# Performance work log

Measured on AMD Instinct MI355X. Metric: run time of the kernel, lower is better.

## Reference

```python
import jax, jax.numpy as jnp
from jax import lax
import numpy as np

LATENT = 256
FLAT = 128 * 28 * 28  # 100352


def _conv(x, w, b, stride):
    # PyTorch Conv2d(k=3, stride, padding=1) in NCHW/OIHW
    y = lax.conv_general_dilated(x, w, (stride, stride), ((1, 1), (1, 1)),
                                 dimension_numbers=('NCHW', 'OIHW', 'NCHW'))
    return y + b[None, :, None, None]


def _deconv(x, w, b):
    # PyTorch ConvTranspose2d(k=3, stride=2, padding=1, output_padding=1).
    # w has PyTorch layout [in, out, kh, kw]; flip spatially + swap io -> OIHW.
    wt = jnp.flip(w, (2, 3)).transpose(1, 0, 2, 3)
    y = lax.conv_general_dilated(x, wt, (1, 1), ((1, 2), (1, 2)),
                                 lhs_dilation=(2, 2),
                                 dimension_numbers=('NCHW', 'OIHW', 'NCHW'))
    return y + b[None, :, None, None]


def _self_attn(x, wq, bq, wk, bk, wv, bv, gamma):
    # Full spatial self-attention over N = H*W tokens (the headroom hotspot).
    B, C, H, W = x.shape
    N = H * W
    xf = x.reshape(B, C, N)
    q = jnp.einsum('oc,bcn->bno', wq, xf) + bq            # [B, N, C//8]
    k = jnp.einsum('oc,bcn->bon', wk, xf) + bk[None, :, None]  # [B, C//8, N]
    attn = jax.nn.softmax(jnp.einsum('bno,bom->bnm', q, k), axis=-1)  # [B,N,N]
    v = jnp.einsum('oc,bcn->bon', wv, xf) + bv[None, :, None]  # [B, C, N]
    out = jnp.einsum('bcn,bmn->bcm', v, attn).reshape(B, C, H, W)
    return gamma * out + x


def setup_inputs() -> dict:
    key = jax.random.key(0)
    ks = iter(jax.random.split(key, 40))
    n = lambda shape, s=0.05: jax.random.normal(next(ks), shape, dtype=jnp.float32) * s
    inp = {
        'x': jax.random.normal(next(ks), (1, 3, 224, 224), dtype=jnp.float32),
        'eps': jax.random.normal(next(ks), (1, LATENT), dtype=jnp.float32),
        'conv1_w': n((32, 3, 3, 3)), 'conv1_b': n((32,)),
        'q1_w': n((4, 32)), 'q1_b': n((4,)),
        'k1_w': n((4, 32)), 'k1_b': n((4,)),
        'v1_w': n((32, 32)), 'v1_b': n((32,)),
        'gamma1': jnp.full((1,), 0.1, dtype=jnp.float32),
        'conv2_w': n((64, 32, 3, 3)), 'conv2_b': n((64,)),
        'q2_w': n((8, 64)), 'q2_b': n((8,)),
        'k2_w': n((8, 64)), 'k2_b': n((8,)),
        'v2_w': n((64, 64)), 'v2_b': n((64,)),
        'gamma2': jnp.full((1,), 0.1, dtype=jnp.float32),
        'conv3_w': n((128, 64, 3, 3)), 'conv3_b': n((128,)),
        'fc_mu_w': n((FLAT, LATENT), 0.01), 'fc_mu_b': n((LATENT,)),
        'fc_lv_w': n((FLAT, LATENT), 0.01), 'fc_lv_b': n((LATENT,)),
        'fc_dec_w': n((LATENT, FLAT), 0.01), 'fc_dec_b': n((FLAT,)),
        'dc1_w': n((128, 64, 3, 3)), 'dc1_b': n((64,)),
        'dc2_w': n((64, 32, 3, 3)), 'dc2_b': n((32,)),
        'dc3_w': n((32, 3, 3, 3)), 'dc3_b': n((3,)),
    }
    return inp


def reference(x, eps, conv1_w, conv1_b, q1_w, q1_b, k1_w, k1_b, v1_w, v1_b, gamma1,
              conv2_w, conv2_b, q2_w, q2_b, k2_w, k2_b, v2_w, v2_b, gamma2,
              conv3_w, conv3_b, fc_mu_w, fc_mu_b, fc_lv_w, fc_lv_b,
              fc_dec_w, fc_dec_b, dc1_w, dc1_b, dc2_w, dc2_b, dc3_w, dc3_b):
    B = x.shape[0]
    h = jax.nn.relu(_conv(x, conv1_w, conv1_b, 2))          # [B,32,112,112]
    h = _self_attn(h, q1_w, q1_b, k1_w, k1_b, v1_w, v1_b, gamma1)
    h = jax.nn.relu(_conv(h, conv2_w, conv2_b, 2))          # [B,64,56,56]
    h = _self_attn(h, q2_w, q2_b, k2_w, k2_b, v2_w, v2_b, gamma2)
    h = jax.nn.relu(_conv(h, conv3_w, conv3_b, 2))          # [B,128,28,28]
    hf = h.reshape(B, FLAT)
    mu = hf @ fc_mu_w + fc_mu_b
    logvar = hf @ fc_lv_w + fc_lv_b
    z = mu + eps * jnp.exp(0.5 * logvar)                    # reparametrize
    d = jax.nn.relu(z @ fc_dec_w + fc_dec_b).reshape(B, 128, 28, 28)
    d = jax.nn.relu(_deconv(d, dc1_w, dc1_b))               # [B,64,56,56]
    d = jax.nn.relu(_deconv(d, dc2_w, dc2_b))               # [B,32,112,112]
    recon = jax.nn.sigmoid(_deconv(d, dc3_w, dc3_b))        # [B,3,224,224]
    return recon, mu, logvar
```

## Files before the change

kernel.cpp:

```cpp
#include <hip/hip_runtime.h>
#include <hip/hip_bf16.h>

typedef __hip_bfloat16 bf16;
typedef __attribute__((ext_vector_type(8))) short short8v;
typedef __attribute__((ext_vector_type(4))) float f32x4;

__device__ __forceinline__ unsigned int cvtpk(float lo, float hi){
  unsigned int r;
  asm volatile("v_cvt_pk_bf16_f32 %0, %1, %2" : "=v"(r) : "v"(lo), "v"(hi));
  return r;
}
__device__ __forceinline__ float exp2a(float x){
  float r;
  asm volatile("v_exp_f32 %0, %1" : "=v"(r) : "v"(x));
  return r;
}

template<int CIN>
__global__ __launch_bounds__(256) void k_conv_s2t(const float* __restrict__ in, const float* __restrict__ w,
    const float* __restrict__ bias, float* __restrict__ out, int Hin, int Win){
  const int Hout = Hin>>1, Wout = Win>>1, HW = Hout*Wout;
  __shared__ float wl[CIN*9];
  const int oc = blockIdx.y, tid = threadIdx.x;
  for(int i=tid;i<CIN*9;i+=256) wl[i] = w[oc*CIN*9 + i];
  __syncthreads();
  const int idx = blockIdx.x*256 + tid;
  if(idx >= HW) return;
  const int oy = idx/Wout, ox = idx - oy*Wout;
  const int iy0 = 2*oy-1, ix0 = 2*ox-1;
  const float mt = iy0>=0 ? 1.f:0.f, ml = ix0>=0 ? 1.f:0.f;
  const int iyc = iy0<0?0:iy0, ixc = ix0<0?0:ix0;
  const int x1 = ix0+1, x2 = ix0+2;
  float acc = bias[oc];
  #pragma unroll 4
  for(int ic=0; ic<CIN; ++ic){
    const float* b0 = in + (ic*Hin + iyc )*Win;
    const float* b1 = in + (ic*Hin + iy0+1)*Win;
    const float* b2 = in + (ic*Hin + iy0+2)*Win;
    const float* wp = wl + ic*9;
    float t00 = b0[ixc]*(mt*ml), t01 = b0[x1]*mt, t02 = b0[x2]*mt;
    float t10 = b1[ixc]*ml,      t11 = b1[x1],    t12 = b1[x2];
    float t20 = b2[ixc]*ml,      t21 = b2[x1],    t22 = b2[x2];
    acc += t00*wp[0]+t01*wp[1]+t02*wp[2]
         + t10*wp[3]+t11*wp[4]+t12*wp[5]
         + t20*wp[6]+t21*wp[7]+t22*wp[8];
  }
  out[oc*HW + idx] = fmaxf(acc, 0.f);
}

template<int C, int O, int TPN>
__global__ __launch_bounds__(256) void k_qkv(const float* __restrict__ x,
    const float* __restrict__ wq, const float* __restrict__ bq,
    const float* __restrict__ wk, const float* __restrict__ bk,
    const float* __restrict__ wv, const float* __restrict__ bv,
    float* __restrict__ q, float* __restrict__ k, bf16* __restrict__ v, int N){
  constexpr int NPB = 256/TPN;
  constexpr int OP = O/TPN > 0 ? O/TPN : 1;
  constexpr int CP = C/TPN;
  const int n = blockIdx.x*NPB + threadIdx.x/TPN;
  const int p = threadIdx.x%TPN;
  float xc[C];
  #pragma unroll
  for(int c=0;c<C;++c) xc[c] = x[c*N+n];
  #pragma unroll
  for(int oo=0;oo<OP;++oo){
    int o = p*OP + oo;
    float aq = bq[o], ak = bk[o];
    #pragma unroll
    for(int c=0;c<C;++c){ aq += wq[o*C+c]*xc[c]; ak += wk[o*C+c]*xc[c]; }
    q[n*O+o] = aq;
    k[o*N+n] = ak;
  }
  #pragma unroll
  for(int cc=0;cc<CP;++cc){
    int o = p*CP + cc;
    float av = bv[o];
    #pragma unroll
    for(int c=0;c<C;++c) av += wv[o*C+c]*xc[c];
    v[o*N+n] = __float2bfloat16(av);
  }
}

template<int C, int O, int ST, int NSPLIT, int QG>
__global__ __launch_bounds__(256) void k_attn_mfma(
    const float* __restrict__ q, const float* __restrict__ kk, const bf16* __restrict__ vb,
    float* __restrict__ pacc, float* __restrict__ pden, int N){
  constexpr int NT = C/16;
  constexpr int OF4 = O/4;
  constexpr int VROW = ST*2 + 16;
  __shared__ __align__(16) char vsm[C*VROW];
  __shared__ float4 ksm4[(ST + ST/8)*OF4];
  const int tid = threadIdx.x;
  const int qblk = blockIdx.x / NSPLIT, split = blockIdx.x % NSPLIT;
  const int KEYS = N / NSPLIT;
  const int kbase = split * KEYS;
  const int wv = tid >> 6;
  const int l  = tid & 63;
  const int lg = l >> 4, lq = l & 15;
  const int qbase = qblk*(64*QG) + wv*(16*QG);
  float qv[QG][O];
  #pragma unroll
  for(int g=0; g<QG; ++g)
    #pragma unroll
    for(int o=0;o<O;++o) qv[g][o] = q[(qbase + g*16 + lq)*O + o] * 1.44269504f;
  f32x4 acc[QG][NT];
  #pragma unroll
  for(int g=0; g<QG; ++g)
    #pragma unroll
    for(int nt=0;nt<NT;++nt) acc[g][nt] = (f32x4){0.f,0.f,0.f,0.f};
  float den[QG];
  #pragma unroll
  for(int g=0; g<QG; ++g) den[g] = 0.f;

  for(int g0=0; g0<KEYS; g0+=ST){
    __syncthreads();
    for(int j=tid; j<ST; j+=256){
      int row = j + (j>>3);
      #pragma unroll
      for(int h=0;h<OF4;++h){
        float4 kv;
        ((float*)&kv)[0] = kk[(h*4+0)*N + kbase + g0 + j];
        ((float*)&kv)[1] = kk[(h*4+1)*N + kbase + g0 + j];
        ((float*)&kv)[2] = kk[(h*4+2)*N + kbase + g0 + j];
        ((float*)&kv)[3] = kk[(h*4+3)*N + kbase + g0 + j];
        ksm4[row*OF4 + h] = kv;
      }
    }
    for(int ch=tid; ch < C*(ST/8); ch += 256){
      int c = ch / (ST/8), j8 = ch % (ST/8);
      *(uint4*)(vsm + c*VROW + j8*16) =
          *(const uint4*)(vb + (size_t)c*N + kbase + g0 + j8*8);
    }
    __syncthreads();
    #pragma unroll
    for(int s=0; s<ST/32; ++s){
      float pr[QG][8];
      #pragma unroll
      for(int e=0; e<8; ++e){
        const int row = s*36 + lg*9 + e;
        #pragma unroll
        for(int g=0; g<QG; ++g){
          float sc = 0.f;
          #pragma unroll
          for(int h=0;h<OF4;++h){
            float4 k4 = ksm4[row*OF4 + h];
            sc += qv[g][h*4+0]*k4.x + qv[g][h*4+1]*k4.y + qv[g][h*4+2]*k4.z + qv[g][h*4+3]*k4.w;
          }
          pr[g][e] = exp2a(sc);
        }
      }
      union { unsigned int u[4]; short8v s8; } pa[QG];
      #pragma unroll
      for(int g=0; g<QG; ++g){
        #pragma unroll
        for(int u=0; u<4; ++u) pa[g].u[u] = cvtpk(pr[g][2*u], pr[g][2*u+1]);
        #pragma unroll
        for(int e=0; e<8; ++e) den[g] += pr[g][e];
      }
      #pragma unroll
      for(int nt=0; nt<NT; ++nt){
        short8v bf_ = *(const short8v*)(vsm + (lq + nt*16)*VROW + (s*32 + lg*8)*2);
        #pragma unroll
        for(int g=0; g<QG; ++g)
          acc[g][nt] = __builtin_amdgcn_mfma_f32_16x16x32_bf16(pa[g].s8, bf_, acc[g][nt], 0,0,0);
      }
    }
  }
  #pragma unroll
  for(int g=0; g<QG; ++g){
    den[g] += __shfl_xor(den[g], 16);
    den[g] += __shfl_xor(den[g], 32);
    if(lg == 0) pden[(size_t)split*N + qbase + g*16 + lq] = den[g];
  }
  #pragma unroll
  for(int g=0; g<QG; ++g)
    #pragma unroll
    for(int nt=0; nt<NT; ++nt)
      #pragma unroll
      for(int r=0;r<4;++r){
        int qg_ = qbase + g*16 + lg*4 + r;
        pacc[((size_t)split*N + qg_)*C + nt*16 + lq] = acc[g][nt][r];
      }
}

template<int C, int NSPLIT>
__global__ __launch_bounds__(256) void k_attn_comb(const float* __restrict__ pacc, const float* __restrict__ pden,
    const float* __restrict__ xin, const float* __restrict__ gamma, float* __restrict__ out, int N){
  int idx = blockIdx.x*256 + threadIdx.x;
  if(idx >= N*C) return;
  int c = idx / N, m = idx - c*N;
  float a = 0.f, d = 0.f;
  #pragma unroll
  for(int s=0;s<NSPLIT;++s){
    a += pacc[((size_t)s*N + m)*C + c];
    d += pden[(size_t)s*N + m];
  }
  out[idx] = gamma[0]*a/d + xin[idx];
}

__global__ __launch_bounds__(256) void k_fc2_part(const float* __restrict__ hf,
    const float* __restrict__ wmu, const float* __restrict__ wlv,
    float* __restrict__ pmu, float* __restrict__ plv){
  __shared__ float sh[64];
  __shared__ float4 red[4][64];
  const int t = threadIdx.x, blk = blockIdx.x, f0 = blk*64;
  const int w = t>>6, l = t&63;
  const float* wsel = blockIdx.y ? wlv : wmu;
  float*       dsel = blockIdx.y ? plv : pmu;
  if(t < 64) sh[t] = hf[f0+t];
  __syncthreads();
  const float4* wp = (const float4*)(wsel + (size_t)(f0 + w*16)*256) + l;
  f32x4 a = {0.f,0.f,0.f,0.f};
  #pragma unroll
  for(int r=0; r<16; ++r){
    float h = sh[w*16 + r];
    float4 u = wp[r*64];
    a[0] += h*u.x; a[1] += h*u.y; a[2] += h*u.z; a[3] += h*u.w;
  }
  red[w][l] = (float4){a[0],a[1],a[2],a[3]};
  __syncthreads();
  const float* rr = (const float*)red;
  dsel[(size_t)blk*256 + t] = rr[t] + rr[256+t] + rr[512+t] + rr[768+t];
}

__global__ __launch_bounds__(256) void k_reparam_p(const float* __restrict__ pmu, const float* __restrict__ plv,
    const float* __restrict__ bmu, const float* __restrict__ blv, const float* __restrict__ eps,
    float* __restrict__ z, float* __restrict__ omu, float* __restrict__ olv){
  const int o = blockIdx.x, t = threadIdx.x;
  __shared__ float rm[4], rl[4];
  float sm = 0.f, sl = 0.f;
  for(int j=t; j<1568; j+=256){ sm += pmu[(size_t)j*256+o]; sl += plv[(size_t)j*256+o]; }
  #pragma unroll
  for(int off=32; off>=1; off>>=1){ sm += __shfl_xor(sm, off); sl += __shfl_xor(sl, off); }
  if((t&63)==0){ rm[t>>6]=sm; rl[t>>6]=sl; }
  __syncthreads();
  if(t==0){
    float mu = bmu[o] + rm[0]+rm[1]+rm[2]+rm[3];
    float lv = blv[o] + rl[0]+rl[1]+rl[2]+rl[3];
    z[o] = mu + eps[o] * expf(0.5f*lv);
    omu[o] = mu;
    olv[o] = lv;
  }
}

template<int OSPL>
__global__ __launch_bounds__(256) void k_fc_dec_p(const float* __restrict__ z, const float* __restrict__ w,
    float* __restrict__ pfd){
  constexpr int OPC = 256/OSPL;
  __shared__ float sz[OPC];
  const int t = threadIdx.x, blk = blockIdx.x, os = blockIdx.y;
  if(t<OPC) sz[t] = z[os*OPC + t];
  __syncthreads();
  const size_t f4 = (size_t)blk*256 + t;
  const float4* wp = (const float4*)w + (size_t)os*OPC*25088 + f4;
  f32x4 a = {0.f,0.f,0.f,0.f};
  #pragma unroll 8
  for(int o=0;o<OPC;++o){
    float zz = sz[o];
    float4 u = wp[(size_t)o*25088];
    a[0] += zz*u.x; a[1] += zz*u.y; a[2] += zz*u.z; a[3] += zz*u.w;
  }
  ((float4*)pfd)[(size_t)os*25088 + f4] = (float4){a[0],a[1],a[2],a[3]};
}

template<int OSPL>
__global__ __launch_bounds__(256) void k_fc_dec_c(const float* __restrict__ pfd, const float* __restrict__ b,
    float* __restrict__ out){
  const int i = blockIdx.x*256 + threadIdx.x;
  const float4* p4 = (const float4*)pfd;
  float4 bb = ((const float4*)b)[i];
  f32x4 s = {bb.x, bb.y, bb.z, bb.w};
  #pragma unroll
  for(int k=0;k<OSPL;++k){
    float4 u = p4[(size_t)k*25088 + i];
    s[0] += u.x; s[1] += u.y; s[2] += u.z; s[3] += u.w;
  }
  ((float4*)out)[i] = (float4){fmaxf(s[0],0.f), fmaxf(s[1],0.f), fmaxf(s[2],0.f), fmaxf(s[3],0.f)};
}

template<int CIN, int COUT, int ACT>
__global__ __launch_bounds__(256) void k_deconv_p(const float* __restrict__ in, const float* __restrict__ w,
    const float* __restrict__ bias, float* __restrict__ out, int Hin, int Win){
  __shared__ float wl[CIN*9];
  const int oc = blockIdx.y;
  const int tid = threadIdx.x;
  for(int i=tid; i<CIN*9; i+=256) wl[i] = w[((i/9)*COUT + oc)*9 + (i%9)];
  __syncthreads();
  const int nq = Hin*Win;
  const int code = blockIdx.x*256 + tid;
  if(code >= 4*nq) return;
  const int q = code % nq;
  const int pcode = code / nq;
  const int px = pcode & 1, py = pcode >> 1;
  const int qy = q / Win, qx = q - qy*Win;
  const float m1x = (qx+1 < Win) ? 1.f : 0.f;
  const float m1y = (qy+1 < Hin) ? 1.f : 0.f;
  const int qxc = (qx+1 < Win) ? qx+1 : qx;
  const int qyc = (qy+1 < Hin) ? qy+1 : qy;
  const int o00 = qy*Win+qx, o01 = qy*Win+qxc, o10 = qyc*Win+qx, o11 = qyc*Win+qxc;
  const int HW = nq;
  float acc = bias[oc];
  if(pcode == 0){
    #pragma unroll 4
    for(int ic=0; ic<CIN; ++ic) acc += in[ic*HW + o00] * wl[ic*9+4];
  } else if(pcode == 1){
    #pragma unroll 4
    for(int ic=0; ic<CIN; ++ic){
      acc += in[ic*HW + o00] * wl[ic*9+5];
      acc += (in[ic*HW + o01]*m1x) * wl[ic*9+3];
    }
  } else if(pcode == 2){
    #pragma unroll 4
    for(int ic=0; ic<CIN; ++ic){
      acc += in[ic*HW + o00] * wl[ic*9+7];
      acc += (in[ic*HW + o10]*m1y) * wl[ic*9+1];
    }
  } else {
    #pragma unroll 4
    for(int ic=0; ic<CIN; ++ic){
      acc += in[ic*HW + o00] * wl[ic*9+8];
      acc += (in[ic*HW + o01]*m1x) * wl[ic*9+6];
      acc += (in[ic*HW + o10]*m1y) * wl[ic*9+2];
      acc += (in[ic*HW + o11]*(m1x*m1y)) * wl[ic*9+0];
    }
  }
  const int oy = 2*qy+py, ox = 2*qx+px;
  float r = (ACT==0) ? fmaxf(acc, 0.f) : 1.f/(1.f + __expf(-acc));
  out[(oc*2*Hin + oy)*2*Win + ox] = r;
}

extern "C" void kernel_launch(void* const* d_in, const int* in_sizes, int n_in,
                              void* d_out, int out_size, void* d_ws, size_t ws_size,
                              hipStream_t stream){
  const float* X    = (const float*)d_in[0];
  const float* EPS  = (const float*)d_in[1];
  const float* c1w  = (const float*)d_in[2];  const float* c1b = (const float*)d_in[3];
  const float* q1w  = (const float*)d_in[4];  const float* q1b = (const float*)d_in[5];
  const float* k1w  = (const float*)d_in[6];  const float* k1b = (const float*)d_in[7];
  const float* v1w  = (const float*)d_in[8];  const float* v1b = (const float*)d_in[9];
  const float* g1   = (const float*)d_in[10];
  const float* c2w  = (const float*)d_in[11]; const float* c2b = (const float*)d_in[12];
  const float* q2w  = (const float*)d_in[13]; const float* q2b = (const float*)d_in[14];
  const float* k2w  = (const float*)d_in[15]; const float* k2b = (const float*)d_in[16];
  const float* v2w  = (const float*)d_in[17]; const float* v2b = (const float*)d_in[18];
  const float* g2   = (const float*)d_in[19];
  const float* c3w  = (const float*)d_in[20]; const float* c3b = (const float*)d_in[21];
  const float* fmw  = (const float*)d_in[22]; const float* fmb = (const float*)d_in[23];
  const float* flw  = (const float*)d_in[24]; const float* flb = (const float*)d_in[25];
  const float* fdw  = (const float*)d_in[26]; const float* fdb = (const float*)d_in[27];
  const float* d1w  = (const float*)d_in[28]; const float* d1b = (const float*)d_in[29];
  const float* d2w  = (const float*)d_in[30]; const float* d2b = (const float*)d_in[31];
  const float* d3w  = (const float*)d_in[32]; const float* d3b = (const float*)d_in[33];

  float* ws  = (float*)d_ws;
  float* h1  = ws;
  float* h1a = h1  + 401408;
  float* q1  = h1a + 401408;
  float* k1  = q1  + 50176;
  float* v1f = k1  + 50176;
  float* h2  = v1f + 401408;
  float* h2a = h2  + 200704;
  float* q2  = h2a + 200704;
  float* k2  = q2  + 25088;
  float* v2f = k2  + 25088;
  float* h3  = v2f + 200704;
  float* z   = h3  + 100352 + 200704;
  float* part= h3  + 100352 + 200704 + 256;
  bf16* v1b_ = (bf16*)v1f;
  bf16* v2b_ = (bf16*)v2f;
  float* pmu = part;
  float* plv = part + 401408;
  float* pfd = part + 802816;
  float* dd0 = h1;
  float* dd1 = h1 + 100352;
  float* dd2 = h1a;

  const size_t base = 2258176;
  const bool big = ws_size >= (base + 2809856 + 87808) * 4;
  float* pdn = part + (big ? 2809856 : 802816);

  float* OUT = (float*)d_out;

  k_conv_s2t<3><<<dim3(49,32),dim3(256),0,stream>>>(X, c1w, c1b, h1, 224, 224);
  k_qkv<32,4,4><<<dim3(196),dim3(256),0,stream>>>(h1, q1w,q1b, k1w,k1b, v1w,v1b, q1,k1,v1b_, 12544);
  if(big){
    k_attn_mfma<32,4,128,7,2><<<dim3(686),dim3(256),0,stream>>>(q1,k1,v1b_, part, pdn, 12544);
    k_attn_comb<32,7><<<dim3(1568),dim3(256),0,stream>>>(part, pdn, h1, g1, h1a, 12544);
  } else {
    k_attn_mfma<32,4,128,2,2><<<dim3(196),dim3(256),0,stream>>>(q1,k1,v1b_, part, pdn, 12544);
    k_attn_comb<32,2><<<dim3(1568),dim3(256),0,stream>>>(part, pdn, h1, g1, h1a, 12544);
  }
  k_conv_s2t<32><<<dim3(13,64),dim3(256),0,stream>>>(h1a, c2w, c2b, h2, 112, 112);
  k_qkv<64,8,8><<<dim3(98),dim3(256),0,stream>>>(h2, q2w,q2b, k2w,k2b, v2w,v2b, q2,k2,v2b_, 3136);
  if(big){
    k_attn_mfma<64,8,64,7,1><<<dim3(343),dim3(256),0,stream>>>(q2,k2,v2b_, part, pdn, 3136);
    k_attn_comb<64,7><<<dim3(784),dim3(256),0,stream>>>(part, pdn, h2, g2, h2a, 3136);
  } else {
    k_attn_mfma<64,8,64,1,1><<<dim3(49),dim3(256),0,stream>>>(q2,k2,v2b_, part, pdn, 3136);
    k_attn_comb<64,1><<<dim3(784),dim3(256),0,stream>>>(part, pdn, h2, g2, h2a, 3136);
  }
  k_conv_s2t<64><<<dim3(4,128),dim3(256),0,stream>>>(h2a, c3w, c3b, h3, 56, 56);
  k_fc2_part<<<dim3(1568,2),dim3(256),0,stream>>>(h3, fmw, flw, pmu, plv);
  k_reparam_p<<<dim3(256),dim3(256),0,stream>>>(pmu, plv, fmb, flb, EPS, z, OUT+150528, OUT+150784);
  if(big){
    k_fc_dec_p<16><<<dim3(98,16),dim3(256),0,stream>>>(z, fdw, pfd);
    k_fc_dec_c<16><<<dim3(98),dim3(256),0,stream>>>(pfd, fdb, dd0);
  } else {
    k_fc_dec_p<4><<<dim3(98,4),dim3(256),0,stream>>>(z, fdw, pfd);
    k_fc_dec_c<4><<<dim3(98),dim3(256),0,stream>>>(pfd, fdb, dd0);
  }
  k_deconv_p<128,64,0><<<dim3(13,64),dim3(256),0,stream>>>(dd0, d1w, d1b, dd1, 28,28);
  k_deconv_p<64,32,0><<<dim3(49,32),dim3(256),0,stream>>>(dd1, d2w, d2b, dd2, 56,56);
  k_deconv_p<32,3,1><<<dim3(196,3),dim3(256),0,stream>>>(dd2, d3w, d3b, OUT, 112,112);
}
```

Before: 390.2 us.

## Double-buffer K/V tiles in attention and transpose combine through shared memory

The attention kernel now prefetches the next K/V tile into registers while the current tile is processed from a second shared-memory buffer, so each tile needs one barrier instead of two and global loads overlap with the MFMA/exp work. The combine kernel is rewritten to read partial accumulators contiguously, transpose them through an LDS tile, and write NCHW output coalesced, replacing the strided gathers. The inline asm also drops `volatile` so the compiler can schedule the exp and convert instructions. The costs are doubled LDS and extra registers held for the prefetch, which may lower occupancy.

```diff
diff --git a/kernel.cpp b/kernel.cpp
--- a/kernel.cpp
+++ b/kernel.cpp
@@ -7,12 +7,12 @@
 
 __device__ __forceinline__ unsigned int cvtpk(float lo, float hi){
   unsigned int r;
-  asm volatile("v_cvt_pk_bf16_f32 %0, %1, %2" : "=v"(r) : "v"(lo), "v"(hi));
+  asm("v_cvt_pk_bf16_f32 %0, %1, %2" : "=v"(r) : "v"(lo), "v"(hi));
   return r;
 }
 __device__ __forceinline__ float exp2a(float x){
   float r;
-  asm volatile("v_exp_f32 %0, %1" : "=v"(r) : "v"(x));
+  asm("v_exp_f32 %0, %1" : "=v"(r) : "v"(x));
   return r;
 }
 
@@ -88,8 +88,9 @@
   constexpr int NT = C/16;
   constexpr int OF4 = O/4;
   constexpr int VROW = ST*2 + 16;
-  __shared__ __align__(16) char vsm[C*VROW];
-  __shared__ float4 ksm4[(ST + ST/8)*OF4];
+  constexpr int VIT  = C*(ST/8)/256;
+  __shared__ __align__(16) char vsm[2][C*VROW];
+  __shared__ float4 ksm4[2][(ST + ST/8)*OF4];
   const int tid = threadIdx.x;
   const int qblk = blockIdx.x / NSPLIT, split = blockIdx.x % NSPLIT;
   const int KEYS = N / NSPLIT;
@@ -112,26 +113,48 @@
   #pragma unroll
   for(int g=0; g<QG; ++g) den[g] = 0.f;
 
-  for(int g0=0; g0<KEYS; g0+=ST){
-    __syncthreads();
-    for(int j=tid; j<ST; j+=256){
-      int row = j + (j>>3);
+  float4 kreg[OF4];
+  uint4  vreg[VIT];
+  const bool kact = tid < ST;
+
+  auto LOAD = [&](int g0){
+    if(kact){
       #pragma unroll
       for(int h=0;h<OF4;++h){
-        float4 kv;
-        ((float*)&kv)[0] = kk[(h*4+0)*N + kbase + g0 + j];
-        ((float*)&kv)[1] = kk[(h*4+1)*N + kbase + g0 + j];
-        ((float*)&kv)[2] = kk[(h*4+2)*N + kbase + g0 + j];
-        ((float*)&kv)[3] = kk[(h*4+3)*N + kbase + g0 + j];
-        ksm4[row*OF4 + h] = kv;
+        ((float*)&kreg[h])[0] = kk[(h*4+0)*N + kbase + g0 + tid];
+        ((float*)&kreg[h])[1] = kk[(h*4+1)*N + kbase + g0 + tid];
+        ((float*)&kreg[h])[2] = kk[(h*4+2)*N + kbase + g0 + tid];
+        ((float*)&kreg[h])[3] = kk[(h*4+3)*N + kbase + g0 + tid];
       }
     }
-    for(int ch=tid; ch < C*(ST/8); ch += 256){
-      int c = ch / (ST/8), j8 = ch % (ST/8);
-      *(uint4*)(vsm + c*VROW + j8*16) =
-          *(const uint4*)(vb + (size_t)c*N + kbase + g0 + j8*8);
-    }
-    __syncthreads();
+    #pragma unroll
+    for(int i=0;i<VIT;++i){
+      int ch = i*256 + tid;
+      int c = ch/(ST/8), j8 = ch%(ST/8);
+      vreg[i] = *(const uint4*)(vb + (size_t)c*N + kbase + g0 + j8*8);
+    }
+  };
+  auto STORE = [&](int b){
+    if(kact){
+      int row = tid + (tid>>3);
+      #pragma unroll
+      for(int h=0;h<OF4;++h) ksm4[b][row*OF4 + h] = kreg[h];
+    }
+    #pragma unroll
+    for(int i=0;i<VIT;++i){
+      int ch = i*256 + tid;
+      int c = ch/(ST/8), j8 = ch%(ST/8);
+      *(uint4*)(vsm[b] + c*VROW + j8*16) = vreg[i];
+    }
+  };
+
+  const int NTILE = KEYS/ST;
+  LOAD(0);
+  STORE(0);
+  __syncthreads();
+  int cur = 0;
+  for(int t=0; t<NTILE; ++t){
+    if(t+1 < NTILE) LOAD((t+1)*ST);
     #pragma unroll
     for(int s=0; s<ST/32; ++s){
       float pr[QG][8];
@@ -143,7 +166,7 @@
           float sc = 0.f;
           #pragma unroll
           for(int h=0;h<OF4;++h){
-            float4 k4 = ksm4[row*OF4 + h];
+            float4 k4 = ksm4[cur][row*OF4 + h];
             sc += qv[g][h*4+0]*k4.x + qv[g][h*4+1]*k4.y + qv[g][h*4+2]*k4.z + qv[g][h*4+3]*k4.w;
           }
           pr[g][e] = exp2a(sc);
@@ -159,12 +182,15 @@
       }
       #pragma unroll
       for(int nt=0; nt<NT; ++nt){
-        short8v bf_ = *(const short8v*)(vsm + (lq + nt*16)*VROW + (s*32 + lg*8)*2);
+        short8v bf_ = *(const short8v*)(vsm[cur] + (lq + nt*16)*VROW + (s*32 + lg*8)*2);
         #pragma unroll
         for(int g=0; g<QG; ++g)
           acc[g][nt] = __builtin_amdgcn_mfma_f32_16x16x32_bf16(pa[g].s8, bf_, acc[g][nt], 0,0,0);
       }
     }
+    if(t+1 < NTILE) STORE(cur^1);
+    __syncthreads();
+    cur ^= 1;
   }
   #pragma unroll
   for(int g=0; g<QG; ++g){
@@ -184,18 +210,38 @@
 }
 
 template<int C, int NSPLIT>
-__global__ __launch_bounds__(256) void k_attn_comb(const float* __restrict__ pacc, const float* __restrict__ pden,
-    const float* __restrict__ xin, const float* __restrict__ gamma, float* __restrict__ out, int N){
-  int idx = blockIdx.x*256 + threadIdx.x;
-  if(idx >= N*C) return;
-  int c = idx / N, m = idx - c*N;
-  float a = 0.f, d = 0.f;
-  #pragma unroll
-  for(int s=0;s<NSPLIT;++s){
-    a += pacc[((size_t)s*N + m)*C + c];
-    d += pden[(size_t)s*N + m];
-  }
-  out[idx] = gamma[0]*a/d + xin[idx];
+__global__ __launch_bounds__(256) void k_attn_combT(const float* __restrict__ pacc,
+    const float* __restrict__ pden, const float* __restrict__ xin,
+    const float* __restrict__ gamma, float* __restrict__ out, int N){
+  __shared__ float tl[C][65];
+  __shared__ float dl[64];
+  const int t = threadIdx.x;
+  const int m0 = blockIdx.x*64;
+  if(t < 64){
+    float d = 0.f;
+    #pragma unroll
+    for(int s=0;s<NSPLIT;++s) d += pden[(size_t)s*N + m0 + t];
+    dl[t] = d;
+  }
+  constexpr int E = 64*C/256;
+  #pragma unroll
+  for(int e=0;e<E;++e){
+    int f = e*256 + t;
+    int ml = f/C, c = f - ml*C;
+    float a = 0.f;
+    #pragma unroll
+    for(int s=0;s<NSPLIT;++s) a += pacc[(size_t)s*N*C + (size_t)m0*C + f];
+    tl[c][ml] = a;
+  }
+  __syncthreads();
+  const float gm = gamma[0];
+  #pragma unroll
+  for(int e=0;e<E;++e){
+    int f = e*256 + t;
+    int c = f>>6, ml = f & 63;
+    size_t gi = (size_t)c*N + m0 + ml;
+    out[gi] = gm * tl[c][ml] / dl[ml] + xin[gi];
+  }
 }
 
 __global__ __launch_bounds__(256) void k_fc2_part(const float* __restrict__ hf,
@@ -385,19 +431,19 @@
   k_qkv<32,4,4><<<dim3(196),dim3(256),0,stream>>>(h1, q1w,q1b, k1w,k1b, v1w,v1b, q1,k1,v1b_, 12544);
   if(big){
     k_attn_mfma<32,4,128,7,2><<<dim3(686),dim3(256),0,stream>>>(q1,k1,v1b_, part, pdn, 12544);
-    k_attn_comb<32,7><<<dim3(1568),dim3(256),0,stream>>>(part, pdn, h1, g1, h1a, 12544);
+    k_attn_combT<32,7><<<dim3(196),dim3(256),0,stream>>>(part, pdn, h1, g1, h1a, 12544);
   } else {
     k_attn_mfma<32,4,128,2,2><<<dim3(196),dim3(256),0,stream>>>(q1,k1,v1b_, part, pdn, 12544);
-    k_attn_comb<32,2><<<dim3(1568),dim3(256),0,stream>>>(part, pdn, h1, g1, h1a, 12544);
+    k_attn_combT<32,2><<<dim3(196),dim3(256),0,stream>>>(part, pdn, h1, g1, h1a, 12544);
   }
   k_conv_s2t<32><<<dim3(13,64),dim3(256),0,stream>>>(h1a, c2w, c2b, h2, 112, 112);
   k_qkv<64,8,8><<<dim3(98),dim3(256),0,stream>>>(h2, q2w,q2b, k2w,k2b, v2w,v2b, q2,k2,v2b_, 3136);
   if(big){
     k_attn_mfma<64,8,64,7,1><<<dim3(343),dim3(256),0,stream>>>(q2,k2,v2b_, part, pdn, 3136);
-    k_attn_comb<64,7><<<dim3(784),dim3(256),0,stream>>>(part, pdn, h2, g2, h2a, 3136);
+    k_attn_combT<64,7><<<dim3(49),dim3(256),0,stream>>>(part, pdn, h2, g2, h2a, 3136);
   } else {
     k_attn_mfma<64,8,64,1,1><<<dim3(49),dim3(256),0,stream>>>(q2,k2,v2b_, part, pdn, 3136);
-    k_attn_comb<64,1><<<dim3(784),dim3(256),0,stream>>>(part, pdn, h2, g2, h2a, 3136);
+    k_attn_combT<64,1><<<dim3(49),dim3(256),0,stream>>>(part, pdn, h2, g2, h2a, 3136);
   }
   k_conv_s2t<64><<<dim3(4,128),dim3(256),0,stream>>>(h2a, c3w, c3b, h3, 56, 56);
   k_fc2_part<<<dim3(1568,2),dim3(256),0,stream>>>(h3, fmw, flw, pmu, plv);
```

New measurement: 351.7 us. 9.9% less time.
